# Performance work log

Hardware: AMD Instinct MI355X
Metric: run time of the kernel (lower is better)

## Reference

```python
import jax, jax.numpy as jnp
import numpy as np

B, S, D, DFF = 8, 2048, 1024, 4096

def setup_inputs() -> dict:
    key = jax.random.key(0)
    ks = jax.random.split(key, 11)
    s = 0.02
    return {
        "x":  jax.random.normal(ks[0], (B, S, D), dtype=jnp.float32),
        "Wq": jax.random.normal(ks[1], (D, D), dtype=jnp.float32) * s,
        "bq": jnp.zeros((D,), dtype=jnp.float32),
        "Wk": jax.random.normal(ks[2], (D, D), dtype=jnp.float32) * s,
        "bk": jnp.zeros((D,), dtype=jnp.float32),
        "Wv": jax.random.normal(ks[3], (D, D), dtype=jnp.float32) * s,
        "bv": jnp.zeros((D,), dtype=jnp.float32),
        "W1": jax.random.normal(ks[4], (DFF, D), dtype=jnp.float32) * s,
        "b1": jnp.zeros((DFF,), dtype=jnp.float32),
        "W2": jax.random.normal(ks[5], (D, DFF), dtype=jnp.float32) * s,
        "b2": jnp.zeros((D,), dtype=jnp.float32),
    }

def reference(x, Wq, bq, Wk, bk, Wv, bv, W1, b1, W2, b2):
    # qkv projections (torch Linear: x @ W.T + b)
    q = jnp.einsum('bsd,ed->bse', x, Wq) + bq
    k = jnp.einsum('bsd,ed->bse', x, Wk) + bk
    v = jnp.einsum('bsd,ed->bse', x, Wv) + bv
    # single-head scaled dot-product attention with causal mask (decoder=True)
    scale = 1.0 / jnp.sqrt(jnp.asarray(q.shape[-1], q.dtype))
    scores = jnp.einsum('bqd,bkd->bqk', q, k) * scale  # (B,S,S)
    causal = jnp.tril(jnp.ones((scores.shape[-2], scores.shape[-1]), dtype=bool))
    scores = jnp.where(causal, scores, jnp.asarray(-jnp.inf, scores.dtype))
    attn = jax.nn.softmax(scores, axis=-1)
    attn_out = jnp.einsum('bqk,bkd->bqd', attn, v)
    # MLP: linear_2(gelu(linear_1(.)))  — exact (erf) GELU as in torch default
    h = jax.nn.gelu(jnp.einsum('bsd,fd->bsf', attn_out, W1) + b1, approximate=False)
    return jnp.einsum('bsf,df->bsd', h, W2) + b2
```

## Files before the change

kernel.cpp:

```cpp
#include <hip/hip_runtime.h>
#include <hip/hip_bf16.h>

#define NB   8
#define SS   2048
#define DD   1024
#define DFFN 4096
#define MTOT (NB*SS)

typedef unsigned short u16;
typedef __attribute__((ext_vector_type(4))) float f32x4;
typedef __attribute__((ext_vector_type(8))) short bf16x8;
typedef __attribute__((ext_vector_type(4))) unsigned short u16x4;
typedef __attribute__((ext_vector_type(8))) unsigned short u16x8;

__device__ __forceinline__ u16 f2bf(float f) {
  union { float f; unsigned u; } c; c.f = f;
  unsigned r = c.u + 0x7FFFu + ((c.u >> 16) & 1u);
  return (u16)(r >> 16);
}

__device__ __forceinline__ void gload16(const void* g, void* l) {
  __builtin_amdgcn_global_load_lds(
      (const __attribute__((address_space(1))) void*)(unsigned long long)g,
      (__attribute__((address_space(3))) void*)(unsigned)(unsigned long long)l,
      16, 0, 0);
}

template<int EBIAS, int EGELU, int ESCALE, int EROWSCALE, int OUTMODE, int ETRANS, int CSKIP, int CK>
__global__ __launch_bounds__(512, 2)
void gemm256(const u16* __restrict__ A, const u16* __restrict__ B,
             const float* __restrict__ bias, const float* __restrict__ rowscale,
             void* __restrict__ C,
             int M, int N, int K, int lda, int ldb, int ldc, float scale,
             long long sA, long long sB, long long sC, int sRS)
{
  __shared__ __align__(1024) u16 smem[65536];

  const int nwg = gridDim.x * gridDim.y;
  const int orig = blockIdx.y * gridDim.x + blockIdx.x;
  const int q = nwg >> 3, r = nwg & 7;
  const int xcd = orig & 7, pos0 = orig >> 3;
  const int wg = (xcd < r ? xcd * (q + 1) : r * (q + 1) + (xcd - r) * q) + pos0;
  const int bx = wg % gridDim.x, by = wg / gridDim.x;
  const int row0 = by * 256, col0 = bx * 256;
  if (CSKIP && col0 > row0 + 255) return;

  const int z = blockIdx.z;
  A += (size_t)z * sA;
  B += (size_t)z * sB;

  int nkt = K >> 5;
  if (CK) { int lim = (row0 + 256) >> 5; if (lim < nkt) nkt = lim; }

  const int tid  = threadIdx.x;
  const int wid  = tid >> 6;
  const int lane = tid & 63;
  const int wr = wid >> 2, wc = wid & 3;

  const int srow = wid * 16 + (lane >> 2);
  const int sunit = (lane & 3) ^ ((lane >> 3) & 3);
  const char* gA = (const char*)A + ((size_t)(row0 + srow) * lda + sunit * 8) * 2;
  const char* gB = (const char*)B + ((size_t)(col0 + srow) * ldb + sunit * 8) * 2;
  char* lbase = (char*)smem;
  const size_t ldab = (size_t)128 * lda * 2;
  const size_t ldbb = (size_t)128 * ldb * 2;

  #define SHA(t2) { char* lb = lbase + ((t2) & 3) * 32768; size_t kb = (size_t)(t2) * 64; \
      gload16(gA + kb,        lb + wid * 1024);                                          \
      gload16(gA + kb + ldab, lb + 8192 + wid * 1024); }
  #define SHB(t2) { char* lb = lbase + ((t2) & 3) * 32768; size_t kb = (size_t)(t2) * 64; \
      gload16(gB + kb,        lb + 16384 + wid * 1024);                                   \
      gload16(gB + kb + ldbb, lb + 16384 + 8192 + wid * 1024); }

  const int fr = lane & 15;
  const int rd_off = fr * 64 + ((lane >> 4) & 3) * 16;
  const int xm = ((lane >> 1) & 3) << 4;
  const int aoff = wr * 8192;
  const int boff = 16384 + wc * 4096;

  f32x4 acc[8][4] = {};
  bf16x8 aLo[4], aHi[4], bb[4];

  SHA(0); SHB(0); SHA(1); SHB(1); SHA(2); SHB(2);
  asm volatile("s_waitcnt vmcnt(8)" ::: "memory");
  asm volatile("s_barrier" ::: "memory");

  for (int t = 0; t < nkt; ++t) {
    const char* cbuf = (const char*)smem + (t & 3) * 32768;
#pragma unroll
    for (int m = 0; m < 4; ++m)
      aLo[m] = *(const bf16x8*)(cbuf + ((aoff + m * 1024 + rd_off) ^ xm));
#pragma unroll
    for (int n = 0; n < 4; ++n)
      bb[n] = *(const bf16x8*)(cbuf + ((boff + n * 1024 + rd_off) ^ xm));
    if (t + 3 < nkt) SHA(t + 3);
    asm volatile("s_barrier" ::: "memory");
    __builtin_amdgcn_s_setprio(1);
#pragma unroll
    for (int m = 0; m < 4; ++m)
#pragma unroll
      for (int n = 0; n < 4; ++n)
        acc[m][n] = __builtin_amdgcn_mfma_f32_16x16x32_bf16(aLo[m], bb[n], acc[m][n], 0, 0, 0);
    __builtin_amdgcn_s_setprio(0);
    asm volatile("s_barrier" ::: "memory");
#pragma unroll
    for (int m = 0; m < 4; ++m)
      aHi[m] = *(const bf16x8*)(cbuf + ((aoff + (m + 4) * 1024 + rd_off) ^ xm));
    if (t + 3 < nkt) SHB(t + 3);
    asm volatile("s_waitcnt vmcnt(8)" ::: "memory");
    asm volatile("s_barrier" ::: "memory");
    __builtin_amdgcn_s_setprio(1);
#pragma unroll
    for (int m = 0; m < 4; ++m)
#pragma unroll
      for (int n = 0; n < 4; ++n)
        acc[m + 4][n] = __builtin_amdgcn_mfma_f32_16x16x32_bf16(aHi[m], bb[n], acc[m + 4][n], 0, 0, 0);
    __builtin_amdgcn_s_setprio(0);
    asm volatile("s_barrier" ::: "memory");
  }
  #undef SHA
  #undef SHB

  asm volatile("s_waitcnt vmcnt(0)" ::: "memory");
  __syncthreads();

  char* sm = (char*)smem;
  const int r4 = (lane >> 4) * 4;

  if (OUTMODE == 1) {
#pragma unroll
    for (int p = 0; p < 2; ++p) {
      if ((wc >> 1) == p) {
#pragma unroll
        for (int n = 0; n < 4; ++n) {
          const int col = col0 + wc * 64 + n * 16 + fr;
          const int pcol = (wc & 1) * 64 + n * 16 + fr;
          float bia = EBIAS ? bias[col] : 0.0f;
#pragma unroll
          for (int m = 0; m < 8; ++m) {
#pragma unroll
            for (int j = 0; j < 4; ++j) {
              const int line = wr * 128 + m * 16 + r4 + j;
              float xv = acc[m][n][j];
              if (EBIAS)     xv += bia;
              if (ESCALE)    xv *= scale;
              if (EROWSCALE) xv *= rowscale[z * sRS + row0 + line];
              if (EGELU)     xv = 0.5f * xv * (1.0f + erff(xv * 0.70710678118f));
              *(float*)(sm + ((line * 512 + pcol * 4) ^ ((line & 12) << 3))) = xv;
            }
          }
        }
      }
      __syncthreads();
      float* Cb = (float*)C + (size_t)z * sC;
#pragma unroll
      for (int i = 0; i < 16; ++i) {
        const int o = i * 8192 + tid * 16;
        const int line = o >> 9, ps = o & 511;
        f32x4 v = *(const f32x4*)(sm + ((line * 512 + ps) ^ ((line & 12) << 3)));
        *(f32x4*)((char*)(Cb + (size_t)(row0 + line) * ldc + col0 + p * 128) + ps) = v;
      }
      __syncthreads();
    }
  } else if (ETRANS) {
#pragma unroll
    for (int n = 0; n < 4; ++n) {
      const int col = col0 + wc * 64 + n * 16 + fr;
      const int line = wc * 64 + n * 16 + fr;
      float bia = EBIAS ? bias[col] : 0.0f;
#pragma unroll
      for (int m = 0; m < 8; ++m) {
        const int rb = wr * 128 + m * 16 + r4;
        u16x4 pk;
#pragma unroll
        for (int j = 0; j < 4; ++j) {
          float xv = acc[m][n][j];
          if (EBIAS)     xv += bia;
          if (ESCALE)    xv *= scale;
          if (EROWSCALE) xv *= rowscale[z * sRS + row0 + rb + j];
          pk[j] = f2bf(xv);
        }
        *(u16x4*)(sm + ((line * 512 + rb * 2) ^ ((line & 15) << 4))) = pk;
      }
    }
    __syncthreads();
    u16* Cb = (u16*)C + (size_t)(row0 >> 11) * (DD * SS) + (row0 & (SS - 1));
#pragma unroll
    for (int i = 0; i < 16; ++i) {
      const int o = i * 8192 + tid * 16;
      const int line = o >> 9, ps = o & 511;
      f32x4 v = *(const f32x4*)(sm + ((line * 512 + ps) ^ ((line & 15) << 4)));
      *(f32x4*)((char*)(Cb + (size_t)(col0 + line) * SS) + ps) = v;
    }
  } else {
#pragma unroll
    for (int n = 0; n < 4; ++n) {
      const int col = col0 + wc * 64 + n * 16 + fr;
      const int pc = (wc * 64 + n * 16 + fr) * 2;
      float bia = EBIAS ? bias[col] : 0.0f;
#pragma unroll
      for (int m = 0; m < 8; ++m) {
#pragma unroll
        for (int j = 0; j < 4; ++j) {
          const int line = wr * 128 + m * 16 + r4 + j;
          float xv = acc[m][n][j];
          if (EBIAS)     xv += bia;
          if (ESCALE)    xv *= scale;
          if (EROWSCALE) xv *= rowscale[z * sRS + row0 + line];
          if (EGELU)     xv = 0.5f * xv * (1.0f + erff(xv * 0.70710678118f));
          u16 u;
          if (OUTMODE == 2) { union { u16 s; _Float16 h; } cu; cu.h = (_Float16)xv; u = cu.s; }
          else u = f2bf(xv);
          *(u16*)(sm + ((line * 512 + pc) ^ ((line & 12) << 3))) = u;
        }
      }
    }
    __syncthreads();
    u16* Cb = (u16*)C + (size_t)z * sC + col0;
#pragma unroll
    for (int i = 0; i < 16; ++i) {
      const int o = i * 8192 + tid * 16;
      const int line = o >> 9, ps = o & 511;
      f32x4 v = *(const f32x4*)(sm + ((line * 512 + ps) ^ ((line & 12) << 3)));
      *(f32x4*)((char*)(Cb + (size_t)(row0 + line) * ldc) + ps) = v;
    }
  }
}

__global__ __launch_bounds__(256) void cvt_bf16_k(const float* __restrict__ in, u16* __restrict__ out, int n4) {
  int i = blockIdx.x * blockDim.x + threadIdx.x;
  if (i < n4) {
    float4 v = ((const float4*)in)[i];
    u16x4 o;
    o.x = f2bf(v.x); o.y = f2bf(v.y); o.z = f2bf(v.z); o.w = f2bf(v.w);
    ((u16x4*)out)[i] = o;
  }
}

__global__ __launch_bounds__(256) void softmax_k(u16* __restrict__ sc, float* __restrict__ rinv, int rows0) {
  const int widx = blockIdx.x * 4 + (threadIdx.x >> 6);
  const int lane = threadIdx.x & 63;
  u16* row = sc + (size_t)widx * SS;
  const int L = (widx & (SS - 1)) + 1;
  float mx = -1e30f;
  for (int k = 0; k < 4; ++k) {
    const int j0 = k * 512 + lane * 8;
    if (j0 < L) {
      u16x8 v = *(const u16x8*)(row + j0);
      int lim = L - j0; if (lim > 8) lim = 8;
#pragma unroll
      for (int e = 0; e < 8; ++e) {
        if (e < lim) { union { u16 u; _Float16 h; } c; c.u = v[e]; mx = fmaxf(mx, (float)c.h); }
      }
    }
  }
#pragma unroll
  for (int o = 32; o >= 1; o >>= 1) mx = fmaxf(mx, __shfl_xor(mx, o));
  float s = 0.0f;
  for (int k = 0; k < 4; ++k) {
    const int j0 = k * 512 + lane * 8;
    u16x8 v = *(const u16x8*)(row + j0);
    u16x8 w;
#pragma unroll
    for (int e = 0; e < 8; ++e) {
      const int j = j0 + e;
      float ev = 0.0f;
      if (j < L) { union { u16 u; _Float16 h; } c; c.u = v[e]; ev = __expf((float)c.h - mx); s += ev; }
      w[e] = f2bf(ev);
    }
    *(u16x8*)(row + j0) = w;
  }
#pragma unroll
  for (int o = 32; o >= 1; o >>= 1) s += __shfl_xor(s, o);
  if (lane == 0) rinv[rows0 + widx] = 1.0f / s;
}

extern "C" void kernel_launch(void* const* d_in, const int* in_sizes, int n_in,
                              void* d_out, int out_size, void* d_ws, size_t ws_size,
                              hipStream_t stream) {
  const float* x  = (const float*)d_in[0];
  const float* Wq = (const float*)d_in[1];
  const float* bq = (const float*)d_in[2];
  const float* Wk = (const float*)d_in[3];
  const float* bk = (const float*)d_in[4];
  const float* Wv = (const float*)d_in[5];
  const float* bv = (const float*)d_in[6];
  const float* W1 = (const float*)d_in[7];
  const float* b1 = (const float*)d_in[8];
  const float* W2 = (const float*)d_in[9];
  const float* b2 = (const float*)d_in[10];

  char* ws = (char*)d_ws;
  u16*  xb   = (u16*)(ws);
  u16*  Wqb  = (u16*)(ws + 33554432);
  u16*  Wkb  = (u16*)(ws + 35651584);
  u16*  Wvb  = (u16*)(ws + 37748736);
  u16*  W1b  = (u16*)(ws + 39845888);
  u16*  W2b  = (u16*)(ws + 48234496);
  u16*  Qb   = (u16*)(ws + 56623104);
  u16*  Kb   = (u16*)(ws + 90177536);
  u16*  Vtb  = (u16*)(ws + 123731968);
  float* rinv = (float*)(ws + 157286400);
  u16*  big  = (u16*)(ws + 157351936);
  u16*  att  = xb;

  const size_t base = 157351936ull;
  const size_t avail = ws_size > base ? ws_size - base : 0;
  int GB = 8; while (GB > 1 && (size_t)GB * 8388608ull > avail) GB >>= 1;
  int MC = 8192; while (MC > 2048 && (size_t)MC * 8192ull > avail) MC >>= 1;

  cvt_bf16_k<<<MTOT * DD / 4 / 256, 256, 0, stream>>>(x, xb, MTOT * DD / 4);
  cvt_bf16_k<<<DD * DD / 4 / 256, 256, 0, stream>>>(Wq, Wqb, DD * DD / 4);
  cvt_bf16_k<<<DD * DD / 4 / 256, 256, 0, stream>>>(Wk, Wkb, DD * DD / 4);
  cvt_bf16_k<<<DD * DD / 4 / 256, 256, 0, stream>>>(Wv, Wvb, DD * DD / 4);
  cvt_bf16_k<<<DFFN * DD / 4 / 256, 256, 0, stream>>>(W1, W1b, DFFN * DD / 4);
  cvt_bf16_k<<<DFFN * DD / 4 / 256, 256, 0, stream>>>(W2, W2b, DFFN * DD / 4);

  gemm256<1,0,0,0,0,0,0,0><<<dim3(DD/256, MTOT/256), 512, 0, stream>>>(
      xb, Wqb, bq, nullptr, (void*)Qb, MTOT, DD, DD, DD, DD, DD, 0.f, 0, 0, 0, 0);
  gemm256<1,0,0,0,0,0,0,0><<<dim3(DD/256, MTOT/256), 512, 0, stream>>>(
      xb, Wkb, bk, nullptr, (void*)Kb, MTOT, DD, DD, DD, DD, DD, 0.f, 0, 0, 0, 0);
  gemm256<1,0,0,0,0,1,0,0><<<dim3(DD/256, MTOT/256), 512, 0, stream>>>(
      xb, Wvb, bv, nullptr, (void*)Vtb, MTOT, DD, DD, DD, DD, DD, 0.f, 0, 0, 0, 0);

  for (int b0 = 0; b0 < NB; b0 += GB) {
    gemm256<0,0,1,0,2,0,1,0><<<dim3(SS/256, SS/256, GB), 512, 0, stream>>>(
        Qb + (size_t)b0 * SS * DD, Kb + (size_t)b0 * SS * DD, nullptr, nullptr,
        (void*)big, SS, SS, DD, DD, DD, SS, 0.03125f,
        (long long)SS * DD, (long long)SS * DD, (long long)SS * SS, 0);
    softmax_k<<<GB * SS / 4, 256, 0, stream>>>(big, rinv, b0 * SS);
    gemm256<0,0,0,1,0,0,0,1><<<dim3(DD/256, SS/256, GB), 512, 0, stream>>>(
        big, Vtb + (size_t)b0 * DD * SS, nullptr, rinv + (size_t)b0 * SS,
        (void*)(att + (size_t)b0 * SS * DD), SS, DD, SS, SS, SS, DD, 0.f,
        (long long)SS * SS, (long long)DD * SS, (long long)SS * DD, SS);
  }

  for (int c = 0; c < MTOT / MC; ++c) {
    u16* h = big;
    gemm256<1,1,0,0,0,0,0,0><<<dim3(DFFN/256, MC/256), 512, 0, stream>>>(
        att + (size_t)c * MC * DD, W1b, b1, nullptr, (void*)h,
        MC, DFFN, DD, DD, DD, DFFN, 0.f, 0, 0, 0, 0);
    gemm256<1,0,0,0,1,0,0,0><<<dim3(DD/256, MC/256), 512, 0, stream>>>(
        h, W2b, b2, nullptr, (void*)((float*)d_out + (size_t)c * MC * DD),
        MC, DD, DFFN, DFFN, DFFN, DD, 0.f, 0, 0, 0, 0);
  }
}
```

Measured before the change: 829.6 us.

## Replace 256x256 GEMM tile with 128x128 double-buffered kernel using inline ds_read

Swaps the 256x256, 512-thread, 4-stage-pipelined GEMM for a 128x128, 256-thread kernel with two LDS buffers, 32KB of LDS and three blocks per CU. LDS fragment reads now go through inline-asm ds_read_b128 and an explicit lgkmcnt wait. The aim is more resident blocks and finer causal-skip granularity. In exchange, each tile reuses less data, so global traffic per FLOP goes up, and the prefetch depth drops from three tiles to one, with a full vmcnt(0) wait every iteration that limits overlap.

Result: faster. 715.4 us (-13.8%).

```diff
diff --git a/kernel.cpp b/kernel.cpp
--- a/kernel.cpp
+++ b/kernel.cpp
@@ -10,6 +10,7 @@
 typedef unsigned short u16;
 typedef __attribute__((ext_vector_type(4))) float f32x4;
 typedef __attribute__((ext_vector_type(8))) short bf16x8;
+typedef __attribute__((ext_vector_type(4))) int i32x4;
 typedef __attribute__((ext_vector_type(4))) unsigned short u16x4;
 typedef __attribute__((ext_vector_type(8))) unsigned short u16x8;
 
@@ -26,15 +27,21 @@
       16, 0, 0);
 }
 
+__device__ __forceinline__ bf16x8 dsr128(unsigned addr) {
+  i32x4 r;
+  asm volatile("ds_read_b128 %0, %1" : "=v"(r) : "v"(addr));
+  return __builtin_bit_cast(bf16x8, r);
+}
+
 template<int EBIAS, int EGELU, int ESCALE, int EROWSCALE, int OUTMODE, int ETRANS, int CSKIP, int CK>
-__global__ __launch_bounds__(512, 2)
-void gemm256(const u16* __restrict__ A, const u16* __restrict__ B,
+__global__ __launch_bounds__(256, 3)
+void gemm128(const u16* __restrict__ A, const u16* __restrict__ B,
              const float* __restrict__ bias, const float* __restrict__ rowscale,
              void* __restrict__ C,
-             int M, int N, int K, int lda, int ldb, int ldc, float scale,
+             int K, int lda, int ldb, int ldc, float scale,
              long long sA, long long sB, long long sC, int sRS)
 {
-  __shared__ __align__(1024) u16 smem[65536];
+  __shared__ __align__(1024) u16 smem[16384];
 
   const int nwg = gridDim.x * gridDim.y;
   const int orig = blockIdx.y * gridDim.x + blockIdx.x;
@@ -42,87 +49,69 @@
   const int xcd = orig & 7, pos0 = orig >> 3;
   const int wg = (xcd < r ? xcd * (q + 1) : r * (q + 1) + (xcd - r) * q) + pos0;
   const int bx = wg % gridDim.x, by = wg / gridDim.x;
-  const int row0 = by * 256, col0 = bx * 256;
-  if (CSKIP && col0 > row0 + 255) return;
+  const int row0 = by * 128, col0 = bx * 128;
+  if (CSKIP && col0 > row0 + 127) return;
 
   const int z = blockIdx.z;
   A += (size_t)z * sA;
   B += (size_t)z * sB;
 
   int nkt = K >> 5;
-  if (CK) { int lim = (row0 + 256) >> 5; if (lim < nkt) nkt = lim; }
+  if (CK) { int lim = (row0 + 128) >> 5; if (lim < nkt) nkt = lim; }
 
   const int tid  = threadIdx.x;
   const int wid  = tid >> 6;
   const int lane = tid & 63;
-  const int wr = wid >> 2, wc = wid & 3;
+  const int wr = wid >> 1, wc = wid & 1;
 
   const int srow = wid * 16 + (lane >> 2);
   const int sunit = (lane & 3) ^ ((lane >> 3) & 3);
   const char* gA = (const char*)A + ((size_t)(row0 + srow) * lda + sunit * 8) * 2;
   const char* gB = (const char*)B + ((size_t)(col0 + srow) * ldb + sunit * 8) * 2;
   char* lbase = (char*)smem;
-  const size_t ldab = (size_t)128 * lda * 2;
-  const size_t ldbb = (size_t)128 * ldb * 2;
-
-  #define SHA(t2) { char* lb = lbase + ((t2) & 3) * 32768; size_t kb = (size_t)(t2) * 64; \
-      gload16(gA + kb,        lb + wid * 1024);                                          \
-      gload16(gA + kb + ldab, lb + 8192 + wid * 1024); }
-  #define SHB(t2) { char* lb = lbase + ((t2) & 3) * 32768; size_t kb = (size_t)(t2) * 64; \
-      gload16(gB + kb,        lb + 16384 + wid * 1024);                                   \
-      gload16(gB + kb + ldbb, lb + 16384 + 8192 + wid * 1024); }
+  const size_t ldab = (size_t)64 * lda * 2;
+  const size_t ldbb = (size_t)64 * ldb * 2;
+
+  #define STG(t2) { char* lb = lbase + ((t2) & 1) * 16384; size_t kb = (size_t)(t2) * 64; \
+      gload16(gA + kb,        lb + wid * 1024);                                           \
+      gload16(gA + kb + ldab, lb + 4096 + wid * 1024);                                    \
+      gload16(gB + kb,        lb + 8192 + wid * 1024);                                    \
+      gload16(gB + kb + ldbb, lb + 8192 + 4096 + wid * 1024); }
 
   const int fr = lane & 15;
-  const int rd_off = fr * 64 + ((lane >> 4) & 3) * 16;
+  const int ks16 = ((lane >> 4) & 3) * 16;
   const int xm = ((lane >> 1) & 3) << 4;
-  const int aoff = wr * 8192;
-  const int boff = 16384 + wc * 4096;
-
-  f32x4 acc[8][4] = {};
-  bf16x8 aLo[4], aHi[4], bb[4];
-
-  SHA(0); SHB(0); SHA(1); SHB(1); SHA(2); SHB(2);
-  asm volatile("s_waitcnt vmcnt(8)" ::: "memory");
+  const unsigned sbase = (unsigned)(unsigned long long)(void*)smem;
+
+  f32x4 acc[4][4] = {};
+
+  STG(0);
+  asm volatile("s_waitcnt vmcnt(0)");
   asm volatile("s_barrier" ::: "memory");
 
   for (int t = 0; t < nkt; ++t) {
-    const char* cbuf = (const char*)smem + (t & 3) * 32768;
+    if (t + 1 < nkt) STG(t + 1);
+    const unsigned cb = sbase + (t & 1) * 16384;
+    bf16x8 af[4], bf[4];
 #pragma unroll
     for (int m = 0; m < 4; ++m)
-      aLo[m] = *(const bf16x8*)(cbuf + ((aoff + m * 1024 + rd_off) ^ xm));
+      af[m] = dsr128(cb + (((wr * 64 + m * 16 + fr) * 64 + ks16) ^ xm));
 #pragma unroll
     for (int n = 0; n < 4; ++n)
-      bb[n] = *(const bf16x8*)(cbuf + ((boff + n * 1024 + rd_off) ^ xm));
-    if (t + 3 < nkt) SHA(t + 3);
+      bf[n] = dsr128(cb + ((8192 + (wc * 64 + n * 16 + fr) * 64 + ks16) ^ xm));
+    asm volatile("s_waitcnt lgkmcnt(0)");
+    __builtin_amdgcn_sched_barrier(0);
+    __builtin_amdgcn_s_setprio(1);
+#pragma unroll
+    for (int m = 0; m < 4; ++m)
+#pragma unroll
+      for (int n = 0; n < 4; ++n)
+        acc[m][n] = __builtin_amdgcn_mfma_f32_16x16x32_bf16(af[m], bf[n], acc[m][n], 0, 0, 0);
+    __builtin_amdgcn_s_setprio(0);
+    asm volatile("s_waitcnt vmcnt(0)");
     asm volatile("s_barrier" ::: "memory");
-    __builtin_amdgcn_s_setprio(1);
-#pragma unroll
-    for (int m = 0; m < 4; ++m)
-#pragma unroll
-      for (int n = 0; n < 4; ++n)
-        acc[m][n] = __builtin_amdgcn_mfma_f32_16x16x32_bf16(aLo[m], bb[n], acc[m][n], 0, 0, 0);
-    __builtin_amdgcn_s_setprio(0);
-    asm volatile("s_barrier" ::: "memory");
-#pragma unroll
-    for (int m = 0; m < 4; ++m)
-      aHi[m] = *(const bf16x8*)(cbuf + ((aoff + (m + 4) * 1024 + rd_off) ^ xm));
-    if (t + 3 < nkt) SHB(t + 3);
-    asm volatile("s_waitcnt vmcnt(8)" ::: "memory");
-    asm volatile("s_barrier" ::: "memory");
-    __builtin_amdgcn_s_setprio(1);
-#pragma unroll
-    for (int m = 0; m < 4; ++m)
-#pragma unroll
-      for (int n = 0; n < 4; ++n)
-        acc[m + 4][n] = __builtin_amdgcn_mfma_f32_16x16x32_bf16(aHi[m], bb[n], acc[m + 4][n], 0, 0, 0);
-    __builtin_amdgcn_s_setprio(0);
-    asm volatile("s_barrier" ::: "memory");
-  }
-  #undef SHA
-  #undef SHB
-
-  asm volatile("s_waitcnt vmcnt(0)" ::: "memory");
-  __syncthreads();
+  }
+  #undef STG
 
   char* sm = (char*)smem;
   const int r4 = (lane >> 4) * 4;
@@ -130,23 +119,23 @@
   if (OUTMODE == 1) {
 #pragma unroll
     for (int p = 0; p < 2; ++p) {
-      if ((wc >> 1) == p) {
+      if (wc == p) {
 #pragma unroll
         for (int n = 0; n < 4; ++n) {
           const int col = col0 + wc * 64 + n * 16 + fr;
-          const int pcol = (wc & 1) * 64 + n * 16 + fr;
+          const int pb = (n * 16 + fr) * 4;
           float bia = EBIAS ? bias[col] : 0.0f;
 #pragma unroll
-          for (int m = 0; m < 8; ++m) {
+          for (int m = 0; m < 4; ++m) {
 #pragma unroll
             for (int j = 0; j < 4; ++j) {
-              const int line = wr * 128 + m * 16 + r4 + j;
+              const int line = wr * 64 + m * 16 + r4 + j;
               float xv = acc[m][n][j];
               if (EBIAS)     xv += bia;
               if (ESCALE)    xv *= scale;
               if (EROWSCALE) xv *= rowscale[z * sRS + row0 + line];
               if (EGELU)     xv = 0.5f * xv * (1.0f + erff(xv * 0.70710678118f));
-              *(float*)(sm + ((line * 512 + pcol * 4) ^ ((line & 12) << 3))) = xv;
+              *(float*)(sm + ((line * 256 + pb) ^ ((line & 7) << 4))) = xv;
             }
           }
         }
@@ -154,11 +143,11 @@
       __syncthreads();
       float* Cb = (float*)C + (size_t)z * sC;
 #pragma unroll
-      for (int i = 0; i < 16; ++i) {
-        const int o = i * 8192 + tid * 16;
-        const int line = o >> 9, ps = o & 511;
-        f32x4 v = *(const f32x4*)(sm + ((line * 512 + ps) ^ ((line & 12) << 3)));
-        *(f32x4*)((char*)(Cb + (size_t)(row0 + line) * ldc + col0 + p * 128) + ps) = v;
+      for (int i = 0; i < 8; ++i) {
+        const int o = i * 4096 + tid * 16;
+        const int line = o >> 8, ps = o & 255;
+        f32x4 v = *(const f32x4*)(sm + ((line * 256 + ps) ^ ((line & 7) << 4)));
+        *(f32x4*)((char*)(Cb + (size_t)(row0 + line) * ldc + col0 + p * 64) + ps) = v;
       }
       __syncthreads();
     }
@@ -169,27 +158,25 @@
       const int line = wc * 64 + n * 16 + fr;
       float bia = EBIAS ? bias[col] : 0.0f;
 #pragma unroll
-      for (int m = 0; m < 8; ++m) {
-        const int rb = wr * 128 + m * 16 + r4;
+      for (int m = 0; m < 4; ++m) {
+        const int rb = wr * 64 + m * 16 + r4;
         u16x4 pk;
 #pragma unroll
         for (int j = 0; j < 4; ++j) {
           float xv = acc[m][n][j];
-          if (EBIAS)     xv += bia;
-          if (ESCALE)    xv *= scale;
-          if (EROWSCALE) xv *= rowscale[z * sRS + row0 + rb + j];
+          if (EBIAS) xv += bia;
           pk[j] = f2bf(xv);
         }
-        *(u16x4*)(sm + ((line * 512 + rb * 2) ^ ((line & 15) << 4))) = pk;
+        *(u16x4*)(sm + ((line * 256 + rb * 2) ^ ((line & 7) << 4))) = pk;
       }
     }
     __syncthreads();
     u16* Cb = (u16*)C + (size_t)(row0 >> 11) * (DD * SS) + (row0 & (SS - 1));
 #pragma unroll
-    for (int i = 0; i < 16; ++i) {
-      const int o = i * 8192 + tid * 16;
-      const int line = o >> 9, ps = o & 511;
-      f32x4 v = *(const f32x4*)(sm + ((line * 512 + ps) ^ ((line & 15) << 4)));
+    for (int i = 0; i < 8; ++i) {
+      const int o = i * 4096 + tid * 16;
+      const int line = o >> 8, ps = o & 255;
+      f32x4 v = *(const f32x4*)(sm + ((line * 256 + ps) ^ ((line & 7) << 4)));
       *(f32x4*)((char*)(Cb + (size_t)(col0 + line) * SS) + ps) = v;
     }
   } else {
@@ -199,10 +186,10 @@
       const int pc = (wc * 64 + n * 16 + fr) * 2;
       float bia = EBIAS ? bias[col] : 0.0f;
 #pragma unroll
-      for (int m = 0; m < 8; ++m) {
+      for (int m = 0; m < 4; ++m) {
 #pragma unroll
         for (int j = 0; j < 4; ++j) {
-          const int line = wr * 128 + m * 16 + r4 + j;
+          const int line = wr * 64 + m * 16 + r4 + j;
           float xv = acc[m][n][j];
           if (EBIAS)     xv += bia;
           if (ESCALE)    xv *= scale;
@@ -211,17 +198,17 @@
           u16 u;
           if (OUTMODE == 2) { union { u16 s; _Float16 h; } cu; cu.h = (_Float16)xv; u = cu.s; }
           else u = f2bf(xv);
-          *(u16*)(sm + ((line * 512 + pc) ^ ((line & 12) << 3))) = u;
+          *(u16*)(sm + ((line * 256 + pc) ^ ((line & 7) << 4))) = u;
         }
       }
     }
     __syncthreads();
     u16* Cb = (u16*)C + (size_t)z * sC + col0;
 #pragma unroll
-    for (int i = 0; i < 16; ++i) {
-      const int o = i * 8192 + tid * 16;
-      const int line = o >> 9, ps = o & 511;
-      f32x4 v = *(const f32x4*)(sm + ((line * 512 + ps) ^ ((line & 12) << 3)));
+    for (int i = 0; i < 8; ++i) {
+      const int o = i * 4096 + tid * 16;
+      const int line = o >> 8, ps = o & 255;
+      f32x4 v = *(const f32x4*)(sm + ((line * 256 + ps) ^ ((line & 7) << 4)));
       *(f32x4*)((char*)(Cb + (size_t)(row0 + line) * ldc) + ps) = v;
     }
   }
@@ -316,32 +303,32 @@
   cvt_bf16_k<<<DFFN * DD / 4 / 256, 256, 0, stream>>>(W1, W1b, DFFN * DD / 4);
   cvt_bf16_k<<<DFFN * DD / 4 / 256, 256, 0, stream>>>(W2, W2b, DFFN * DD / 4);
 
-  gemm256<1,0,0,0,0,0,0,0><<<dim3(DD/256, MTOT/256), 512, 0, stream>>>(
-      xb, Wqb, bq, nullptr, (void*)Qb, MTOT, DD, DD, DD, DD, DD, 0.f, 0, 0, 0, 0);
-  gemm256<1,0,0,0,0,0,0,0><<<dim3(DD/256, MTOT/256), 512, 0, stream>>>(
-      xb, Wkb, bk, nullptr, (void*)Kb, MTOT, DD, DD, DD, DD, DD, 0.f, 0, 0, 0, 0);
-  gemm256<1,0,0,0,0,1,0,0><<<dim3(DD/256, MTOT/256), 512, 0, stream>>>(
-      xb, Wvb, bv, nullptr, (void*)Vtb, MTOT, DD, DD, DD, DD, DD, 0.f, 0, 0, 0, 0);
+  gemm128<1,0,0,0,0,0,0,0><<<dim3(DD/128, MTOT/128), 256, 0, stream>>>(
+      xb, Wqb, bq, nullptr, (void*)Qb, DD, DD, DD, DD, 0.f, 0, 0, 0, 0);
+  gemm128<1,0,0,0,0,0,0,0><<<dim3(DD/128, MTOT/128), 256, 0, stream>>>(
+      xb, Wkb, bk, nullptr, (void*)Kb, DD, DD, DD, DD, 0.f, 0, 0, 0, 0);
+  gemm128<1,0,0,0,0,1,0,0><<<dim3(DD/128, MTOT/128), 256, 0, stream>>>(
+      xb, Wvb, bv, nullptr, (void*)Vtb, DD, DD, DD, DD, 0.f, 0, 0, 0, 0);
 
   for (int b0 = 0; b0 < NB; b0 += GB) {
-    gemm256<0,0,1,0,2,0,1,0><<<dim3(SS/256, SS/256, GB), 512, 0, stream>>>(
+    gemm128<0,0,1,0,2,0,1,0><<<dim3(SS/128, SS/128, GB), 256, 0, stream>>>(
         Qb + (size_t)b0 * SS * DD, Kb + (size_t)b0 * SS * DD, nullptr, nullptr,
-        (void*)big, SS, SS, DD, DD, DD, SS, 0.03125f,
+        (void*)big, DD, DD, DD, SS, 0.03125f,
         (long long)SS * DD, (long long)SS * DD, (long long)SS * SS, 0);
     softmax_k<<<GB * SS / 4, 256, 0, stream>>>(big, rinv, b0 * SS);
-    gemm256<0,0,0,1,0,0,0,1><<<dim3(DD/256, SS/256, GB), 512, 0, stream>>>(
+    gemm128<0,0,0,1,0,0,0,1><<<dim3(DD/128, SS/128, GB), 256, 0, stream>>>(
         big, Vtb + (size_t)b0 * DD * SS, nullptr, rinv + (size_t)b0 * SS,
-        (void*)(att + (size_t)b0 * SS * DD), SS, DD, SS, SS, SS, DD, 0.f,
+        (void*)(att + (size_t)b0 * SS * DD), SS, SS, SS, DD, 0.f,
         (long long)SS * SS, (long long)DD * SS, (long long)SS * DD, SS);
   }
 
   for (int c = 0; c < MTOT / MC; ++c) {
     u16* h = big;
-    gemm256<1,1,0,0,0,0,0,0><<<dim3(DFFN/256, MC/256), 512, 0, stream>>>(
+    gemm128<1,1,0,0,0,0,0,0><<<dim3(DFFN/128, MC/128), 256, 0, stream>>>(
         att + (size_t)c * MC * DD, W1b, b1, nullptr, (void*)h,
-        MC, DFFN, DD, DD, DD, DFFN, 0.f, 0, 0, 0, 0);
-    gemm256<1,0,0,0,1,0,0,0><<<dim3(DD/256, MC/256), 512, 0, stream>>>(
+        DD, DD, DD, DFFN, 0.f, 0, 0, 0, 0);
+    gemm128<1,0,0,0,1,0,0,0><<<dim3(DD/128, MC/128), 256, 0, stream>>>(
         h, W2b, b2, nullptr, (void*)((float*)d_out + (size_t)c * MC * DD),
-        MC, DD, DFFN, DFFN, DFFN, DD, 0.f, 0, 0, 0, 0);
-  }
-}
+        DFFN, DFFN, DFFN, DD, 0.f, 0, 0, 0, 0);
+  }
+}
```
